# Optimization experiments

Measured on AMD Instinct MI355X. Metric: run time of the kernel, lower is better.

Reference implementation:

```python
import jax, jax.numpy as jnp
import numpy as np

N = 4096        # atoms
F = 128         # node feature channels (MACE hidden irreps scalar channels)
K = 8           # radial basis size
NELEM = 10      # chemical elements
RMAX = 5.0      # cutoff (Angstrom), model.r_max
BOX = 34.5      # box side -> ~0.1 atoms/A^3, ~50 neighbors within RMAX


def setup_inputs() -> dict:
    key = jax.random.key(0)
    ks = jax.random.split(key, 7)
    positions = jax.random.uniform(ks[0], (N, 3), jnp.float32) * BOX
    z = jax.random.randint(ks[1], (N,), 0, NELEM)
    embed = jax.random.normal(ks[2], (NELEM, F), jnp.float32) * 0.1
    W1 = jax.random.normal(ks[3], (K, F, F), jnp.float32) / np.sqrt(K * F)
    W2 = jax.random.normal(ks[4], (K, F, F), jnp.float32) / np.sqrt(K * F)
    Wr1 = jax.random.normal(ks[5], (F, F), jnp.float32) / np.sqrt(F)
    Wr2 = jax.random.normal(ks[6], (F, 1), jnp.float32) / np.sqrt(F)
    return dict(positions=positions, z=z, embed=embed, W1=W1, W2=W2, Wr1=Wr1, Wr2=Wr2)


def _energy(positions, embed, W1, W2, Wr1, Wr2, z):
    # node embedding from atomic species (node_attrs one-hot @ embedding)
    h = embed[z]                                            # [N,F]
    # --- neighborlist: radius graph with self-edge masking (pbc = False) ---
    sq = jnp.sum(positions * positions, axis=-1)            # [N]
    d2 = sq[:, None] + sq[None, :] - 2.0 * (positions @ positions.T)  # [N,N]
    eye = jnp.eye(positions.shape[0], dtype=bool)
    d2_safe = jnp.where(eye | (d2 <= 0), 1.0, d2)           # avoid sqrt(0) grad
    d = jnp.sqrt(d2_safe)                                   # [N,N]
    mask = (d < RMAX) & (~eye) & (d2 > 0)                   # keep_edge = ~true_self_edge
    # smooth cutoff envelope
    env = jnp.where(mask, 0.5 * (jnp.cos(jnp.pi * d / RMAX) + 1.0), 0.0)  # [N,N]
    # Gaussian radial basis
    mus = jnp.linspace(0.0, RMAX, K, dtype=jnp.float32)     # [K]
    gamma = jnp.float32((K / RMAX) ** 2)
    rbf = jnp.exp(-gamma * (d[..., None] - mus) ** 2) * env[..., None]    # [N,N,K]
    # --- two message-passing layers (radial-weighted neighbor aggregation) ---
    for W in (W1, W2):
        A = jnp.einsum('ijk,jf->ikf', rbf, h)               # [N,K,F] gather-scatter agg
        h = jax.nn.silu(jnp.einsum('ikf,kfg->ig', A, W) + h)  # [N,F]
    # --- per-atom energy readout, summed over graph ---
    e_atom = (jax.nn.silu(h @ Wr1) @ Wr2)[:, 0]             # [N]
    return jnp.sum(e_atom)


def reference(positions, z, embed, W1, W2, Wr1, Wr2):
    energy, dE_dpos = jax.value_and_grad(_energy)(positions, embed, W1, W2, Wr1, Wr2, z)
    forces = -dE_dpos                                       # [N,3]
    return energy, forces
```

## Files before the change

### kernel.cpp

```cpp
#include <hip/hip_runtime.h>
#include <math.h>

#define N_ATOMS 4096
#define F 128
#define K 8
#define KF 1024
#define KFF 131072
#define FF 16384
#define NF 524288
#define NKF 4194304
#define MAXNB 128
#define RMAX 5.0f
#define RMAX2 25.0f
#define GAMMA 2.56f
#define MU_STEP 0.714285714285714f
#define PI_F 3.14159265358979323846f
#define POR (PI_F / RMAX)

typedef __bf16 bf16x8_t __attribute__((ext_vector_type(8)));
typedef float f32x4_t __attribute__((ext_vector_type(4)));
typedef unsigned short u16x8_t __attribute__((ext_vector_type(8)));
typedef unsigned short u16x4_t __attribute__((ext_vector_type(4)));

__device__ __forceinline__ float sigm(float x){ return 1.0f/(1.0f + expf(-x)); }
__device__ __forceinline__ unsigned short f2bf(float x){
  unsigned int u = __float_as_uint(x);
  u += 0x7fff + ((u >> 16) & 1);
  return (unsigned short)(u >> 16);
}


__device__ __forceinline__ void agg_body(int a, int t,
        const unsigned short* __restrict__ h_in, const int* __restrict__ nb_idx,
        const float* __restrict__ rbf, const int* __restrict__ nb_cnt,
        unsigned short* __restrict__ Af){
  int grp = t >> 6, lane = t & 63;
  __shared__ int s_j[MAXNB];
  __shared__ float s_acc[4][8][128];
  int cnt = nb_cnt[a];
  for (int idx = t; idx < cnt; idx += 256) s_j[idx] = nb_idx[a*MAXNB + idx];
  __syncthreads();
  float2 acc[8];
  #pragma unroll
  for (int k = 0; k < 8; k++) acc[k] = {0.f, 0.f};
  const float4* rb = (const float4*)(rbf + (size_t)a*MAXNB*8);
  for (int n = grp; n < cnt; n += 4){
    unsigned int pv = *(const unsigned int*)&h_in[(size_t)s_j[n]*F + lane*2];
    float hx = __uint_as_float(pv << 16);
    float hy = __uint_as_float(pv & 0xffff0000u);
    float4 r0 = rb[n*2], r1 = rb[n*2+1];
    acc[0].x += r0.x*hx; acc[0].y += r0.x*hy;
    acc[1].x += r0.y*hx; acc[1].y += r0.y*hy;
    acc[2].x += r0.z*hx; acc[2].y += r0.z*hy;
    acc[3].x += r0.w*hx; acc[3].y += r0.w*hy;
    acc[4].x += r1.x*hx; acc[4].y += r1.x*hy;
    acc[5].x += r1.y*hx; acc[5].y += r1.y*hy;
    acc[6].x += r1.z*hx; acc[6].y += r1.z*hy;
    acc[7].x += r1.w*hx; acc[7].y += r1.w*hy;
  }
  #pragma unroll
  for (int k = 0; k < 8; k++)
    *(float2*)&s_acc[grp][k][lane*2] = acc[k];
  __syncthreads();
  int k = t >> 5, q = t & 31;
  int f0 = q*4;
  float v[4];
  #pragma unroll
  for (int i = 0; i < 4; i++){
    int f = f0 + i;
    v[i] = s_acc[0][k][f] + s_acc[1][k][f] + s_acc[2][k][f] + s_acc[3][k][f];
  }
  int lf = (a & 15) | (((f0 >> 3) & 3) << 4);
  int kc = k*4 + (f0 >> 5);
  size_t flat = (size_t)(a >> 4)*16384 + ((size_t)kc*64 + lf)*8 + (f0 & 7);
  u16x4_t o;
  o[0] = f2bf(v[0]); o[1] = f2bf(v[1]); o[2] = f2bf(v[2]); o[3] = f2bf(v[3]);
  *(u16x4_t*)(Af + flat) = o;
}

__device__ __forceinline__ void mgemm_bwd_body(int bx, int t,
        const unsigned short* __restrict__ Gf, const unsigned short* __restrict__ Bf,
        unsigned short* __restrict__ dAbf){
  int l = t & 63, w = t >> 6;
  int rtile = (bx & 63)*4 + w;
  int nt0 = (bx >> 6)*8;
  f32x4_t acc[8];
  #pragma unroll
  for (int i = 0; i < 8; i++) acc[i] = (f32x4_t){0.f,0.f,0.f,0.f};
  const unsigned short* Ab = Gf + (size_t)rtile*2048 + l*8;
  const unsigned short* Bb = Bf + l*8;
  #pragma unroll
  for (int kc = 0; kc < 4; kc++){
    bf16x8_t a = *(const bf16x8_t*)(Ab + kc*512);
    #pragma unroll
    for (int nt = 0; nt < 8; nt++){
      bf16x8_t b = *(const bf16x8_t*)(Bb + (kc*64 + nt0 + nt)*512);
      acc[nt] = __builtin_amdgcn_mfma_f32_16x16x32_bf16(a, b, acc[nt], 0, 0, 0);
    }
  }
  int row0 = rtile*16 + (l >> 4)*4;
  int col = l & 15;
  #pragma unroll
  for (int nt = 0; nt < 8; nt++){
    #pragma unroll
    for (int r = 0; r < 4; r++)
      dAbf[(size_t)(row0+r)*1024 + (nt0+nt)*16 + col] = f2bf(acc[nt][r]);
  }
}


__global__ __launch_bounds__(256) void k_prep(const float* __restrict__ pos,
        const int* __restrict__ z, const float* __restrict__ embed,
        const float* __restrict__ W1, const float* __restrict__ W2,
        const float* __restrict__ Wr1,
        int* __restrict__ nb_idx, float* __restrict__ nb_d, int* __restrict__ nb_cnt,
        float* __restrict__ rbf, float* __restrict__ drbf,
        unsigned short* __restrict__ WF1, unsigned short* __restrict__ WF2,
        unsigned short* __restrict__ WDF2, unsigned short* __restrict__ WTF1,
        unsigned short* __restrict__ WTF2, unsigned short* __restrict__ Wr1F,
        unsigned short* __restrict__ Wr1TF,
        float* __restrict__ h0, unsigned short* __restrict__ h0bf){
  int t = threadIdx.x;
  if (blockIdx.x < 2048){
    int w2 = t >> 7;
    int half = (t >> 6) & 1;
    int lane = t & 63;
    int i = blockIdx.x*2 + w2;
    __shared__ float spx[2][256], spy[2][256], spz[2][256], ssq[2][256];
    __shared__ int s_jl[2][2][128];
    __shared__ float s_dl[2][2][128];
    __shared__ int s_cnt[2][2];
    float pix = pos[3*i], piy = pos[3*i+1], piz = pos[3*i+2];
    float sqi = pix*pix + piy*piy + piz*piz;
    int count = 0;
    for (int it = 0; it < 8; it++){
      __syncthreads();
      {
        int j0 = it*256 + t;
        float px = pos[3*j0], py = pos[3*j0+1], pz = pos[3*j0+2];
        spx[0][t] = px; spy[0][t] = py; spz[0][t] = pz;
        ssq[0][t] = px*px + py*py + pz*pz;
        int j1 = 2048 + it*256 + t;
        px = pos[3*j1]; py = pos[3*j1+1]; pz = pos[3*j1+2];
        spx[1][t] = px; spy[1][t] = py; spz[1][t] = pz;
        ssq[1][t] = px*px + py*py + pz*pz;
      }
      __syncthreads();
      #pragma unroll
      for (int c = 0; c < 4; c++){
        int jj = c*64 + lane;
        int j = half*2048 + it*256 + jj;
        float dot = pix*spx[half][jj] + piy*spy[half][jj] + piz*spz[half][jj];
        float d2 = sqi + ssq[half][jj] - 2.0f*dot;
        bool pred = (j != i) && (d2 > 0.0f) && (d2 < RMAX2);
        unsigned long long m = __ballot(pred);
        int off = __popcll(m & ((1ull << lane) - 1ull));
        if (pred){
          int p = count + off;
          if (p < 128){ s_jl[w2][half][p] = j; s_dl[w2][half][p] = sqrtf(d2); }
        }
        count += __popcll(m);
      }
    }
    if (lane == 0) s_cnt[w2][half] = count;
    __syncthreads();
    int c0 = s_cnt[w2][0]; if (c0 > 128) c0 = 128;
    int c1 = s_cnt[w2][1]; if (c1 > 128) c1 = 128;
    int cc = c0 + c1; if (cc > MAXNB) cc = MAXNB;
    int tia = t & 127;
    if (tia == 0) nb_cnt[i] = cc;
    for (int n = tia; n < cc; n += 128){
      int j; float d;
      if (n < c0){ j = s_jl[w2][0][n]; d = s_dl[w2][0][n]; }
      else       { j = s_jl[w2][1][n - c0]; d = s_dl[w2][1][n - c0]; }
      nb_idx[i*MAXNB + n] = j;
      nb_d[i*MAXNB + n] = d;
      float ph = POR*d;
      float cph, sph;
      __sincosf(ph, &sph, &cph);
      float env = 0.5f*(cph + 1.0f);
      float denv = -0.5f*POR*sph;
      float rr[8], dd[8];
      #pragma unroll
      for (int k = 0; k < 8; k++){
        float dm = d - MU_STEP*(float)k;
        float G = expf(-GAMMA*dm*dm);
        rr[k] = G*env;
        dd[k] = G*(-2.0f*GAMMA*dm*env + denv);
      }
      float4* rb = (float4*)(rbf + ((size_t)i*MAXNB + n)*8);
      rb[0] = {rr[0],rr[1],rr[2],rr[3]};
      rb[1] = {rr[4],rr[5],rr[6],rr[7]};
      float4* db = (float4*)(drbf + ((size_t)i*MAXNB + n)*8);
      db[0] = {dd[0],dd[1],dd[2],dd[3]};
      db[1] = {dd[4],dd[5],dd[6],dd[7]};
    }
    return;
  }
  if (blockIdx.x >= 2112){
    int idx = (blockIdx.x - 2112)*256 + t;
    int i = idx >> 7, f = idx & 127;
    float v = embed[z[i]*F + f];
    h0[idx] = v;
    h0bf[idx] = f2bf(v);
    return;
  }
  int idx = (blockIdx.x - 2048)*256 + t;
  int l = idx & 63;
  int hi = idx >> 6;
  {
    int kc = hi >> 3, nt = hi & 7;
    int kfb = kc*32 + ((l>>4)&3)*8;
    int g = nt*16 + (l&15);
    u16x8_t v1, v2, vd;
    #pragma unroll
    for (int j = 0; j < 8; j++){
      int kf = kfb + j;
      v1[j] = f2bf(W1[kf*128 + g]);
      v2[j] = f2bf(W2[kf*128 + g]);
      vd[j] = f2bf(W2[(kf>>7)*FF + g*F + (kf&127)]);
    }
    *(u16x8_t*)(WF1 + idx*8) = v1;
    *(u16x8_t*)(WF2 + idx*8) = v2;
    *(u16x8_t*)(WDF2 + idx*8) = vd;
  }
  {
    int kc = hi >> 6, nt = hi & 63;
    int gb = kc*32 + ((l>>4)&3)*8;
    int kf = nt*16 + (l&15);
    u16x8_t t1, t2;
    #pragma unroll
    for (int j = 0; j < 8; j++){
      int g = gb + j;
      t1[j] = f2bf(W1[kf*128 + g]);
      t2[j] = f2bf(W2[kf*128 + g]);
    }
    *(u16x8_t*)(WTF1 + idx*8) = t1;
    *(u16x8_t*)(WTF2 + idx*8) = t2;
  }
  {
    int m = idx >> 9;
    int ll = (idx >> 3) & 63;
    int j = idx & 7;
    int kc = m >> 3, nt = m & 7;
    int kf = kc*32 + ((ll>>4)&3)*8 + j;
    int g = nt*16 + (ll&15);
    Wr1F[idx]  = f2bf(Wr1[kf*128 + g]);
    Wr1TF[idx] = f2bf(Wr1[g*128 + kf]);
  }
}

__global__ __launch_bounds__(256) void k_agg(const unsigned short* __restrict__ h_in,
        const int* __restrict__ nb_idx, const float* __restrict__ rbf,
        const int* __restrict__ nb_cnt, unsigned short* __restrict__ Af){
  agg_body(blockIdx.x, threadIdx.x, h_in, nb_idx, rbf, nb_cnt, Af);
}

__global__ __launch_bounds__(256) void k_bwdmix(const unsigned short* __restrict__ Gf,
        const unsigned short* __restrict__ Bf, unsigned short* __restrict__ dAbf,
        const unsigned short* __restrict__ g2bf, const int* __restrict__ nb_idx,
        const float* __restrict__ rbf, const int* __restrict__ nb_cnt,
        unsigned short* __restrict__ Af){
  if (blockIdx.x < 512){
    mgemm_bwd_body(blockIdx.x, threadIdx.x, Gf, Bf, dAbf);
    return;
  }
  agg_body(blockIdx.x - 512, threadIdx.x, g2bf, nb_idx, rbf, nb_cnt, Af);
}

__global__ __launch_bounds__(256) void k_mgemm_bwd(const unsigned short* __restrict__ Gf,
        const unsigned short* __restrict__ Bf, unsigned short* __restrict__ dAbf){
  mgemm_bwd_body(blockIdx.x, threadIdx.x, Gf, Bf, dAbf);
}

__global__ __launch_bounds__(256) void k_mgemm_fwd(const unsigned short* __restrict__ Af,
        const unsigned short* __restrict__ Bf, const float* __restrict__ addv,
        const float* __restrict__ msrc, float* __restrict__ out_m,
        float* __restrict__ out_h, unsigned short* __restrict__ out_hbf,
        unsigned short* __restrict__ out_frag, int mode){
  int t = threadIdx.x;
  int l = t & 63, w = t >> 6;
  int rtile = blockIdx.x;
  int nt = blockIdx.y*4 + w;
  f32x4_t accA = (f32x4_t){0.f,0.f,0.f,0.f};
  f32x4_t accB = (f32x4_t){0.f,0.f,0.f,0.f};
  const unsigned short* Ab = Af + (size_t)rtile*16384 + l*8;
  const unsigned short* Bb = Bf + l*8;
  #pragma unroll
  for (int kc = 0; kc < 32; kc += 2){
    bf16x8_t a0 = *(const bf16x8_t*)(Ab + kc*512);
    bf16x8_t b0 = *(const bf16x8_t*)(Bb + (kc*8 + nt)*512);
    bf16x8_t a1 = *(const bf16x8_t*)(Ab + (kc+1)*512);
    bf16x8_t b1 = *(const bf16x8_t*)(Bb + ((kc+1)*8 + nt)*512);
    accA = __builtin_amdgcn_mfma_f32_16x16x32_bf16(a0, b0, accA, 0, 0, 0);
    accB = __builtin_amdgcn_mfma_f32_16x16x32_bf16(a1, b1, accB, 0, 0, 0);
  }
  f32x4_t acc = accA + accB;
  int row0 = rtile*16 + (l >> 4)*4;
  int col = nt*16 + (l & 15);
  if (mode == 0){
    #pragma unroll
    for (int r = 0; r < 4; r++){
      int i = row0 + r;
      float m = acc[r] + addv[(size_t)i*F + col];
      out_m[(size_t)i*F + col] = m;
      float h = m*sigm(m);
      out_h[(size_t)i*F + col] = h;
      out_hbf[(size_t)i*F + col] = f2bf(h);
    }
  } else {
    int kc2 = col >> 5;
    int lfr0 = (((col >> 3) & 3) << 4);
    int jj = col & 7;
    #pragma unroll
    for (int r = 0; r < 4; r++){
      int i = row0 + r;
      float mm = msrc[(size_t)i*F + col];
      float sg = sigm(mm);
      float gv = (acc[r] + addv[(size_t)i*F + col])*(sg*(1.f + mm*(1.f - sg)));
      int lfr = (i & 15) | lfr0;
      size_t flat = (((size_t)(i>>4)*4 + kc2)*64 + lfr)*8 + jj;
      out_frag[flat] = f2bf(gv);
    }
  }
}

__global__ __launch_bounds__(64) void k_readout(const unsigned short* __restrict__ h2bf,
        const float* __restrict__ m2, const unsigned short* __restrict__ Wr1F,
        const unsigned short* __restrict__ Wr1TF, const float* __restrict__ Wr2,
        float* __restrict__ e_at, float* __restrict__ g2,
        unsigned short* __restrict__ g2bf, unsigned short* __restrict__ g2frag){
  int a0 = blockIdx.x*16;
  int l = threadIdx.x;
  int rl = l & 15;
  __shared__ unsigned short sdu[16][136];
  f32x4_t acc[8];
  #pragma unroll
  for (int nt = 0; nt < 8; nt++) acc[nt] = (f32x4_t){0.f,0.f,0.f,0.f};
  #pragma unroll
  for (int kc = 0; kc < 4; kc++){
    bf16x8_t af = *(const bf16x8_t*)(h2bf + (size_t)(a0+rl)*F + kc*32 + ((l>>4)&3)*8);
    #pragma unroll
    for (int nt = 0; nt < 8; nt++){
      bf16x8_t bf = *(const bf16x8_t*)(Wr1F + ((kc*8+nt)*64 + l)*8);
      acc[nt] = __builtin_amdgcn_mfma_f32_16x16x32_bf16(af, bf, acc[nt], 0, 0, 0);
    }
  }
  float epart[4] = {0.f,0.f,0.f,0.f};
  #pragma unroll
  for (int nt = 0; nt < 8; nt++){
    float w2 = Wr2[nt*16 + rl];
    #pragma unroll
    for (int r = 0; r < 4; r++){
      float u = acc[nt][r];
      float sg = sigm(u);
      epart[r] += u*sg*w2;
      sdu[(l>>4)*4 + r][nt*16 + rl] = f2bf(w2*(sg*(1.f + u*(1.f - sg))));
    }
  }
  #pragma unroll
  for (int o = 1; o < 16; o <<= 1){
    #pragma unroll
    for (int r = 0; r < 4; r++) epart[r] += __shfl_xor(epart[r], o);
  }
  if (rl == 0){
    #pragma unroll
    for (int r = 0; r < 4; r++) e_at[a0 + (l>>4)*4 + r] = epart[r];
  }
  __syncthreads();
  f32x4_t acc2[8];
  #pragma unroll
  for (int nt = 0; nt < 8; nt++) acc2[nt] = (f32x4_t){0.f,0.f,0.f,0.f};
  #pragma unroll
  for (int kc = 0; kc < 4; kc++){
    bf16x8_t af = *(const bf16x8_t*)&sdu[rl][kc*32 + ((l>>4)&3)*8];
    #pragma unroll
    for (int nt = 0; nt < 8; nt++){
      bf16x8_t bf = *(const bf16x8_t*)(Wr1TF + ((kc*8+nt)*64 + l)*8);
      acc2[nt] = __builtin_amdgcn_mfma_f32_16x16x32_bf16(af, bf, acc2[nt], 0, 0, 0);
    }
  }
  #pragma unroll
  for (int nt = 0; nt < 8; nt++){
    int g = nt*16 + rl;
    int kc2 = g >> 5;
    int lfr0 = (((g >> 3) & 3) << 4);
    int jj = g & 7;
    #pragma unroll
    for (int r = 0; r < 4; r++){
      int a = a0 + (l>>4)*4 + r;
      float mm = m2[(size_t)a*F + g];
      float sg = sigm(mm);
      float gv = acc2[nt][r]*(sg*(1.f + mm*(1.f - sg)));
      g2[(size_t)a*F + g] = gv;
      unsigned short gb = f2bf(gv);
      g2bf[(size_t)a*F + g] = gb;
      int lfr = (a & 15) | lfr0;
      g2frag[(((size_t)(a>>4)*4 + kc2)*64 + lfr)*8 + jj] = gb;
    }
  }
}

__global__ __launch_bounds__(256) void k_edge(const unsigned short* __restrict__ dA2bf,
        const unsigned short* __restrict__ dA1bf, const unsigned short* __restrict__ h1bf,
        const unsigned short* __restrict__ h0bf, const float* __restrict__ drbf,
        const int* __restrict__ nb_idx, const int* __restrict__ nb_cnt,
        float* __restrict__ edge_s){
  int a = blockIdx.x;
  int t = threadIdx.x;
  int w = t >> 6, l = t & 63;
  __shared__ int s_j[MAXNB];
  int cnt = nb_cnt[a];
  for (int idx = t; idx < cnt; idx += 256) s_j[idx] = nb_idx[a*MAXNB + idx];
  int r = l & 15;
  int sel = (l >> 4) & 3;
  u16x8_t a2u[4], a1u[4];
  #pragma unroll
  for (int kc = 0; kc < 4; kc++){
    u16x8_t v2 = {0,0,0,0,0,0,0,0};
    u16x8_t v1 = {0,0,0,0,0,0,0,0};
    if (r < 8){
      v2 = *(const u16x8_t*)(dA2bf + (size_t)a*KF + r*F + kc*32 + sel*8);
      v1 = *(const u16x8_t*)(dA1bf + (size_t)a*KF + r*F + kc*32 + sel*8);
    }
    a2u[kc] = v2; a1u[kc] = v1;
  }
  __syncthreads();
  for (int n0 = w*16; n0 < cnt; n0 += 64){
    int nl = n0 + r;
    int nls = nl < cnt ? nl : cnt - 1;
    int j = s_j[nls];
    const unsigned short* h1p = h1bf + (size_t)j*F + sel*8;
    const unsigned short* h0p = h0bf + (size_t)j*F + sel*8;
    f32x4_t acc = (f32x4_t){0.f,0.f,0.f,0.f};
    #pragma unroll
    for (int kc = 0; kc < 4; kc++){
      bf16x8_t b = *(const bf16x8_t*)(h1p + kc*32);
      acc = __builtin_amdgcn_mfma_f32_16x16x32_bf16(*(const bf16x8_t*)&a2u[kc], b, acc, 0, 0, 0);
    }
    #pragma unroll
    for (int kc = 0; kc < 4; kc++){
      bf16x8_t b = *(const bf16x8_t*)(h0p + kc*32);
      acc = __builtin_amdgcn_mfma_f32_16x16x32_bf16(*(const bf16x8_t*)&a1u[kc], b, acc, 0, 0, 0);
    }
    int krow = (l >> 4) * 4;
    float part = 0.f;
    if (krow < 8){
      float4 dr = *(const float4*)(drbf + ((size_t)a*MAXNB + nls)*8 + krow);
      part = acc[0]*dr.x + acc[1]*dr.y + acc[2]*dr.z + acc[3]*dr.w;
    }
    part += __shfl_xor(part, 16);
    if (l < 16 && nl < cnt) edge_s[a*MAXNB + nl] = part;
  }
}

__global__ __launch_bounds__(256) void k_force(const float* __restrict__ pos,
        const int* __restrict__ nb_idx, const float* __restrict__ nb_d,
        const int* __restrict__ nb_cnt, const float* __restrict__ edge_s,
        const float* __restrict__ e_at, float* __restrict__ out){
  int bw = threadIdx.x >> 6, lane = threadIdx.x & 63;
  if (blockIdx.x == N_ATOMS/4){
    if (bw == 0){
      float s = 0.f;
      for (int i = lane; i < N_ATOMS; i += 64) s += e_at[i];
      #pragma unroll
      for (int o = 1; o < 64; o <<= 1) s += __shfl_xor(s, o);
      if (lane == 0) out[0] = s;
    }
    return;
  }
  int a = blockIdx.x*4 + bw;
  float pax = pos[3*a], pay = pos[3*a+1], paz = pos[3*a+2];
  int cnt = nb_cnt[a];
  float fx = 0.f, fy = 0.f, fz = 0.f;
  for (int n = lane; n < cnt; n += 64){
    int j = nb_idx[a*MAXNB + n];
    float d = nb_d[a*MAXNB + n];
    float s = edge_s[a*MAXNB + n];
    int cj = nb_cnt[j];
    int lo = 0, hi = cj - 1, p = -1;
    while (lo <= hi){
      int mid = (lo + hi) >> 1;
      int v = nb_idx[j*MAXNB + mid];
      if (v == a){ p = mid; break; }
      if (v < a) lo = mid + 1; else hi = mid - 1;
    }
    float sj = (p >= 0) ? edge_s[j*MAXNB + p] : 0.0f;
    float coef = (s + sj)/d;
    float dx = pax - pos[3*j], dy = pay - pos[3*j+1], dz = paz - pos[3*j+2];
    fx -= coef*dx; fy -= coef*dy; fz -= coef*dz;
  }
  #pragma unroll
  for (int o = 1; o < 64; o <<= 1){
    fx += __shfl_xor(fx, o); fy += __shfl_xor(fy, o); fz += __shfl_xor(fz, o);
  }
  if (lane == 0){
    out[1 + 3*a + 0] = fx;
    out[1 + 3*a + 1] = fy;
    out[1 + 3*a + 2] = fz;
  }
}

extern "C" void kernel_launch(void* const* d_in, const int* in_sizes, int n_in,
                              void* d_out, int out_size, void* d_ws, size_t ws_size,
                              hipStream_t stream){
  const float* pos   = (const float*)d_in[0];
  const int*   z     = (const int*)  d_in[1];
  const float* embed = (const float*)d_in[2];
  const float* W1    = (const float*)d_in[3];
  const float* W2    = (const float*)d_in[4];
  const float* Wr1   = (const float*)d_in[5];
  const float* Wr2   = (const float*)d_in[6];
  float* out = (float*)d_out;

  float* ws = (float*)d_ws;
  float* h0   = ws;
  float* h1   = h0 + NF;
  float* h2   = h1 + NF;
  float* m1   = h2 + NF;
  float* m2   = m1 + NF;
  float* g2b  = m2 + NF;
  float* Bbuf = g2b + NF;
  float* Cbuf = Bbuf + NKF;
  unsigned short* dA2bf = (unsigned short*)Bbuf;
  unsigned short* dA1bf = (unsigned short*)Cbuf;
  unsigned short* Afrag = (unsigned short*)(Cbuf + NKF);
  unsigned short* Gfrag = Afrag + NKF;
  unsigned short* h0bf = Gfrag + NF;
  unsigned short* h1bf = h0bf + NF;
  unsigned short* h2bf = h1bf + NF;
  unsigned short* g2bf = h2bf + NF;
  unsigned short* WF1  = g2bf + NF;
  unsigned short* WF2  = WF1 + KFF;
  unsigned short* WDF2 = WF2 + KFF;
  unsigned short* WTF1 = WDF2 + KFF;
  unsigned short* WTF2 = WTF1 + KFF;
  unsigned short* Wr1F  = WTF2 + KFF;
  unsigned short* Wr1TF = Wr1F + FF;
  float* e_at = (float*)(Wr1TF + FF);
  float* nb_d = e_at + N_ATOMS;
  float* edge_s = nb_d + N_ATOMS*MAXNB;
  float* rbf  = edge_s + N_ATOMS*MAXNB;
  float* drbf = rbf + N_ATOMS*MAXNB*8;
  int* nb_idx = (int*)(drbf + N_ATOMS*MAXNB*8);
  int* nb_cnt = nb_idx + N_ATOMS*MAXNB;

  k_prep<<<2048 + 64 + NF/256, 256, 0, stream>>>(pos, z, embed, W1, W2, Wr1,
        nb_idx, nb_d, nb_cnt, rbf, drbf,
        WF1, WF2, WDF2, WTF1, WTF2, Wr1F, Wr1TF, h0, h0bf);

  k_agg<<<N_ATOMS, 256, 0, stream>>>(h0bf, nb_idx, rbf, nb_cnt, Afrag);
  k_mgemm_fwd<<<dim3(256, 2), 256, 0, stream>>>(Afrag, WF1, h0, h0, m1, h1, h1bf, Gfrag, 0);
  k_agg<<<N_ATOMS, 256, 0, stream>>>(h1bf, nb_idx, rbf, nb_cnt, Afrag);
  k_mgemm_fwd<<<dim3(256, 2), 256, 0, stream>>>(Afrag, WF2, h1, h1, m2, h2, h2bf, Gfrag, 0);

  k_readout<<<N_ATOMS/16, 64, 0, stream>>>(h2bf, m2, Wr1F, Wr1TF, Wr2, e_at, g2b, g2bf, Gfrag);

  k_bwdmix<<<512 + N_ATOMS, 256, 0, stream>>>(Gfrag, WTF2, dA2bf,
        g2bf, nb_idx, rbf, nb_cnt, Afrag);
  k_mgemm_fwd<<<dim3(256, 2), 256, 0, stream>>>(Afrag, WDF2, g2b, m1, m1, m1, h2bf, Gfrag, 1);
  k_mgemm_bwd<<<512, 256, 0, stream>>>(Gfrag, WTF1, dA1bf);
  k_edge<<<N_ATOMS, 256, 0, stream>>>(dA2bf, dA1bf, h1bf, h0bf, drbf, nb_idx, nb_cnt, edge_s);
  k_force<<<N_ATOMS/4 + 1, 256, 0, stream>>>(pos, nb_idx, nb_d, nb_cnt, edge_s, e_at, out);
}
```

Before: 187.3 us.

## Fuse layer-1 backward gradient GEMM with dA1 GEMM via shared memory

```diff
diff --git a/kernel.cpp b/kernel.cpp
--- a/kernel.cpp
+++ b/kernel.cpp
@@ -268,16 +268,70 @@
   agg_body(blockIdx.x - 512, threadIdx.x, g2bf, nb_idx, rbf, nb_cnt, Af);
 }
 
-__global__ __launch_bounds__(256) void k_mgemm_bwd(const unsigned short* __restrict__ Gf,
-        const unsigned short* __restrict__ Bf, unsigned short* __restrict__ dAbf){
-  mgemm_bwd_body(blockIdx.x, threadIdx.x, Gf, Bf, dAbf);
+__global__ __launch_bounds__(256) void k_g1dA1(const unsigned short* __restrict__ Af,
+        const unsigned short* __restrict__ WDF2, const float* __restrict__ g2b,
+        const float* __restrict__ m1, const unsigned short* __restrict__ WTF1,
+        unsigned short* __restrict__ dA1bf){
+  int t = threadIdx.x;
+  int l = t & 63, w = t >> 6;
+  int rtile = blockIdx.x;
+  __shared__ unsigned short sG[2048];
+  const unsigned short* Ab = Af + (size_t)rtile*16384 + l*8;
+  #pragma unroll
+  for (int q = 0; q < 2; q++){
+    int nt = w*2 + q;
+    f32x4_t accA = (f32x4_t){0.f,0.f,0.f,0.f};
+    f32x4_t accB = (f32x4_t){0.f,0.f,0.f,0.f};
+    const unsigned short* Bb = WDF2 + l*8;
+    #pragma unroll
+    for (int kc = 0; kc < 32; kc += 2){
+      bf16x8_t a0 = *(const bf16x8_t*)(Ab + kc*512);
+      bf16x8_t b0 = *(const bf16x8_t*)(Bb + (kc*8 + nt)*512);
+      bf16x8_t a1 = *(const bf16x8_t*)(Ab + (kc+1)*512);
+      bf16x8_t b1 = *(const bf16x8_t*)(Bb + ((kc+1)*8 + nt)*512);
+      accA = __builtin_amdgcn_mfma_f32_16x16x32_bf16(a0, b0, accA, 0, 0, 0);
+      accB = __builtin_amdgcn_mfma_f32_16x16x32_bf16(a1, b1, accB, 0, 0, 0);
+    }
+    f32x4_t acc = accA + accB;
+    int row0 = (l >> 4)*4;
+    int col = nt*16 + (l & 15);
+    int kc2 = col >> 5;
+    int lfr0 = (((col >> 3) & 3) << 4);
+    int jj = col & 7;
+    #pragma unroll
+    for (int r = 0; r < 4; r++){
+      int i = rtile*16 + row0 + r;
+      float mm = m1[(size_t)i*F + col];
+      float sg = sigm(mm);
+      float gv = (acc[r] + g2b[(size_t)i*F + col])*(sg*(1.f + mm*(1.f - sg)));
+      int lfr = ((row0 + r) & 15) | lfr0;
+      sG[(kc2*64 + lfr)*8 + jj] = f2bf(gv);
+    }
+  }
+  __syncthreads();
+  bf16x8_t ag[4];
+  #pragma unroll
+  for (int kc = 0; kc < 4; kc++) ag[kc] = *(const bf16x8_t*)&sG[(kc*64 + l)*8];
+  int row0 = rtile*16 + (l >> 4)*4;
+  int col = l & 15;
+  for (int ntt = 0; ntt < 16; ntt++){
+    int nt = w*16 + ntt;
+    f32x4_t acc = (f32x4_t){0.f,0.f,0.f,0.f};
+    #pragma unroll
+    for (int kc = 0; kc < 4; kc++){
+      bf16x8_t b = *(const bf16x8_t*)(WTF1 + ((kc*64 + nt)*64 + l)*8);
+      acc = __builtin_amdgcn_mfma_f32_16x16x32_bf16(ag[kc], b, acc, 0, 0, 0);
+    }
+    #pragma unroll
+    for (int r = 0; r < 4; r++)
+      dA1bf[(size_t)(row0+r)*1024 + nt*16 + col] = f2bf(acc[r]);
+  }
 }
 
 __global__ __launch_bounds__(256) void k_mgemm_fwd(const unsigned short* __restrict__ Af,
         const unsigned short* __restrict__ Bf, const float* __restrict__ addv,
-        const float* __restrict__ msrc, float* __restrict__ out_m,
-        float* __restrict__ out_h, unsigned short* __restrict__ out_hbf,
-        unsigned short* __restrict__ out_frag, int mode){
+        float* __restrict__ out_m, float* __restrict__ out_h,
+        unsigned short* __restrict__ out_hbf){
   int t = threadIdx.x;
   int l = t & 63, w = t >> 6;
   int rtile = blockIdx.x;
@@ -298,30 +352,14 @@
   f32x4_t acc = accA + accB;
   int row0 = rtile*16 + (l >> 4)*4;
   int col = nt*16 + (l & 15);
-  if (mode == 0){
-    #pragma unroll
-    for (int r = 0; r < 4; r++){
-      int i = row0 + r;
-      float m = acc[r] + addv[(size_t)i*F + col];
-      out_m[(size_t)i*F + col] = m;
-      float h = m*sigm(m);
-      out_h[(size_t)i*F + col] = h;
-      out_hbf[(size_t)i*F + col] = f2bf(h);
-    }
-  } else {
-    int kc2 = col >> 5;
-    int lfr0 = (((col >> 3) & 3) << 4);
-    int jj = col & 7;
-    #pragma unroll
-    for (int r = 0; r < 4; r++){
-      int i = row0 + r;
-      float mm = msrc[(size_t)i*F + col];
-      float sg = sigm(mm);
-      float gv = (acc[r] + addv[(size_t)i*F + col])*(sg*(1.f + mm*(1.f - sg)));
-      int lfr = (i & 15) | lfr0;
-      size_t flat = (((size_t)(i>>4)*4 + kc2)*64 + lfr)*8 + jj;
-      out_frag[flat] = f2bf(gv);
-    }
+  #pragma unroll
+  for (int r = 0; r < 4; r++){
+    int i = row0 + r;
+    float m = acc[r] + addv[(size_t)i*F + col];
+    out_m[(size_t)i*F + col] = m;
+    float h = m*sigm(m);
+    out_h[(size_t)i*F + col] = h;
+    out_hbf[(size_t)i*F + col] = f2bf(h);
   }
 }
 
@@ -550,16 +588,15 @@
         WF1, WF2, WDF2, WTF1, WTF2, Wr1F, Wr1TF, h0, h0bf);
 
   k_agg<<<N_ATOMS, 256, 0, stream>>>(h0bf, nb_idx, rbf, nb_cnt, Afrag);
-  k_mgemm_fwd<<<dim3(256, 2), 256, 0, stream>>>(Afrag, WF1, h0, h0, m1, h1, h1bf, Gfrag, 0);
+  k_mgemm_fwd<<<dim3(256, 2), 256, 0, stream>>>(Afrag, WF1, h0, m1, h1, h1bf);
   k_agg<<<N_ATOMS, 256, 0, stream>>>(h1bf, nb_idx, rbf, nb_cnt, Afrag);
-  k_mgemm_fwd<<<dim3(256, 2), 256, 0, stream>>>(Afrag, WF2, h1, h1, m2, h2, h2bf, Gfrag, 0);
+  k_mgemm_fwd<<<dim3(256, 2), 256, 0, stream>>>(Afrag, WF2, h1, m2, h2, h2bf);
 
   k_readout<<<N_ATOMS/16, 64, 0, stream>>>(h2bf, m2, Wr1F, Wr1TF, Wr2, e_at, g2b, g2bf, Gfrag);
 
   k_bwdmix<<<512 + N_ATOMS, 256, 0, stream>>>(Gfrag, WTF2, dA2bf,
         g2bf, nb_idx, rbf, nb_cnt, Afrag);
-  k_mgemm_fwd<<<dim3(256, 2), 256, 0, stream>>>(Afrag, WDF2, g2b, m1, m1, m1, h2bf, Gfrag, 1);
-  k_mgemm_bwd<<<512, 256, 0, stream>>>(Gfrag, WTF1, dA1bf);
+  k_g1dA1<<<256, 256, 0, stream>>>(Afrag, WDF2, g2b, m1, WTF1, dA1bf);
   k_edge<<<N_ATOMS, 256, 0, stream>>>(dA2bf, dA1bf, h1bf, h0bf, drbf, nb_idx, nb_cnt, edge_s);
   k_force<<<N_ATOMS/4 + 1, 256, 0, stream>>>(pos, nb_idx, nb_d, nb_cnt, edge_s, e_at, out);
 }
```

Result: no change. 189.7 us (+1.2%).
